# Optimization experiments

Hardware: AMD Instinct MI355X
Metric: run time of the kernel (lower is better)

## Reference

```python
import jax, jax.numpy as jnp
import numpy as np

N_NODES = 100000
N_EDGES = 1600000
IN_DIM, HIDDEN, OUT_DIM = 128, 64, 32
LN_EPS = 1e-5


def setup_inputs() -> dict:
    key = jax.random.key(0)
    ks = jax.random.split(key, 12)
    x = jax.random.normal(ks[0], (N_NODES, IN_DIM), dtype=jnp.float32)
    edge_index = jax.random.randint(ks[1], (2, N_EDGES), 0, N_NODES, dtype=jnp.int64)
    s = 1.0 / np.sqrt(IN_DIM)
    s2 = 1.0 / np.sqrt(HIDDEN)
    return {
        "x": x,
        "edge_index": edge_index,
        "W_self0": jax.random.uniform(ks[2], (IN_DIM, HIDDEN), jnp.float32, -s, s),
        "W_neigh0": jax.random.uniform(ks[3], (IN_DIM, HIDDEN), jnp.float32, -s, s),
        "b0": jnp.zeros((HIDDEN,), jnp.float32),
        "g0": jnp.ones((HIDDEN,), jnp.float32),
        "be0": jnp.zeros((HIDDEN,), jnp.float32),
        "W_self1": jax.random.uniform(ks[4], (HIDDEN, OUT_DIM), jnp.float32, -s2, s2),
        "W_neigh1": jax.random.uniform(ks[5], (HIDDEN, OUT_DIM), jnp.float32, -s2, s2),
        "b1": jnp.zeros((OUT_DIM,), jnp.float32),
        "g1": jnp.ones((OUT_DIM,), jnp.float32),
        "be1": jnp.zeros((OUT_DIM,), jnp.float32),
    }


def _sage_layer(h, src, dst, W_self, W_neigh, b, g, be):
    n = h.shape[0]
    # mean aggregation of neighbor features via scatter-add + count
    agg = jax.ops.segment_sum(h[src], dst, num_segments=n)  # [N, F]
    cnt = jax.ops.segment_sum(jnp.ones((src.shape[0],), h.dtype), dst, num_segments=n)
    agg = agg / jnp.clip(cnt, 1.0)[:, None]
    z = h @ W_self + agg @ W_neigh + b  # [N, out]
    mu = jnp.mean(z, axis=-1, keepdims=True)
    var = jnp.mean((z - mu) ** 2, axis=-1, keepdims=True)
    zn = (z - mu) * jax.lax.rsqrt(var + LN_EPS) * g + be
    return jax.nn.relu(zn)


def reference(x, edge_index, W_self0, W_neigh0, b0, g0, be0,
              W_self1, W_neigh1, b1, g1, be1):
    src, dst = edge_index[0], edge_index[1]
    h = _sage_layer(x, src, dst, W_self0, W_neigh0, b0, g0, be0)
    h = _sage_layer(h, src, dst, W_self1, W_neigh1, b1, g1, be1)
    return h
```

## Files before the change

### kernel.cpp

```cpp
#include <hip/hip_runtime.h>
#include <hip/hip_bf16.h>

#define N_NODES 100000
#define N_EDGES 1600000
#define IN_DIM 128
#define HID 64
#define OUT_DIM 32
#define LN_EPS 1e-5f
#define NBKT 782
#define NPBLK 500
#define PAIRS_PER_BLK 1600
#define G0T 1563
#define PADCAP 384

typedef __attribute__((ext_vector_type(8))) _Float16 half8;
typedef __attribute__((ext_vector_type(8))) short short8;
typedef __attribute__((ext_vector_type(4))) float f32x4;

__device__ __forceinline__ float uflo(unsigned int u) {
  return __uint_as_float(u << 16);
}
__device__ __forceinline__ float ufhi(unsigned int u) {
  return __uint_as_float(u & 0xffff0000u);
}
__device__ __forceinline__ unsigned short bf16rne(float f) {
  unsigned int u = __float_as_uint(f);
  unsigned int r = u + 0x7fffu + ((u >> 16) & 1u);
  return (unsigned short)(r >> 16);
}
__device__ __forceinline__ unsigned int pk(float lo, float hi) {
  return (unsigned int)bf16rne(lo) | ((unsigned int)bf16rne(hi) << 16);
}

__global__ void detect_edges(const int* __restrict__ w, int* __restrict__ flag,
                             unsigned short* __restrict__ p0u,
                             unsigned short* __restrict__ p1u) {
  __shared__ int any;
  if (threadIdx.x == 0) any = 0;
  __syncthreads();
  if (w[2 * threadIdx.x + 1] != 0) any = 1;
  __syncthreads();
  if (threadIdx.x == 0) flag[0] = any ? 0 : 1;
  const int t = threadIdx.x;
  if (t < HID) p0u[(size_t)N_NODES * HID + t] = 0;
  if (t < OUT_DIM) p1u[(size_t)N_NODES * OUT_DIM + t] = 0;
}

__global__ __launch_bounds__(256) void convW(
    const float* __restrict__ Wn0, const float* __restrict__ Ws0,
    const float* __restrict__ Wn1, const float* __restrict__ Ws1,
    _Float16* __restrict__ B0f, unsigned short* __restrict__ B1u) {
  const int i = blockIdx.x * 256 + threadIdx.x;
  if (i < 128 * 128) {
    const int n = i >> 7, k = i & 127;
    const float w = (n < 64) ? Wn0[k * 64 + n] : Ws0[k * 64 + (n - 64)];
    B0f[i] = (_Float16)w;
  } else if (i < 128 * 128 + 64 * 64) {
    const int j = i - 128 * 128;
    const int n = j >> 6, k = j & 63;
    const float w = (n < 32) ? Wn1[k * 32 + n] : Ws1[k * 32 + (n - 32)];
    B1u[j] = bf16rne(w);
  }
}

__device__ __forceinline__ void gemm0_body(
    int rowblk, int colgrp, int tid, _Float16* lb,
    const float* __restrict__ x, const _Float16* __restrict__ B0f,
    const float* __restrict__ b0, unsigned short* __restrict__ p0u,
    unsigned short* __restrict__ s0bu) {
  const int lane = tid & 63;
  const int wave = tid >> 6;
  const int rowbase = rowblk * 64 + wave * 16;
  const int arow = rowbase + (lane & 15);
  const int rclamp = (arow < N_NODES) ? arow : 0;
  const int ko = (lane >> 4) << 3;

  float av[32];
  {
    const float* ax = x + (size_t)rclamp * IN_DIM + ko;
#pragma unroll
    for (int ks = 0; ks < 4; ++ks) {
      *(float4*)&av[ks * 8] = *(const float4*)(ax + ks * 32);
      *(float4*)&av[ks * 8 + 4] = *(const float4*)(ax + ks * 32 + 4);
    }
  }
  {
    const uint4* gsrc = (const uint4*)(B0f + (colgrp << 13));
    for (int i = tid; i < 1024; i += 256) {
      const int o = i << 4;
      const int sw = o ^ (((o >> 8) & 7) << 4);
      *(uint4*)((char*)lb + sw) = gsrc[i];
    }
  }
  __syncthreads();

  half8 ah[4];
#pragma unroll
  for (int ks = 0; ks < 4; ++ks) {
#pragma unroll
    for (int j = 0; j < 8; ++j) ah[ks][j] = (_Float16)av[ks * 8 + j];
  }

  f32x4 acc[4];
#pragma unroll
  for (int ct = 0; ct < 4; ++ct) acc[ct] = (f32x4){0.f, 0.f, 0.f, 0.f};

#pragma unroll
  for (int ks = 0; ks < 4; ++ks) {
    const int kb = ks * 64 + (ko << 1);
#pragma unroll
    for (int ct = 0; ct < 4; ++ct) {
      const int n = ct * 16 + (lane & 15);
      const int boff = (n << 8) + kb;
      const int sb = boff ^ (((boff >> 8) & 7) << 4);
      const half8 bv = *(const half8*)((const char*)lb + sb);
      acc[ct] = __builtin_amdgcn_mfma_f32_16x16x32_f16(ah[ks], bv, acc[ct], 0, 0, 0);
    }
  }
  const int rb4 = rowbase + ((lane >> 4) << 2);
  const int cc = lane & 15;
  if (colgrp == 0) {
#pragma unroll
    for (int ct = 0; ct < 4; ++ct) {
#pragma unroll
      for (int j = 0; j < 4; ++j) {
        const int r = rb4 + j;
        if (r < N_NODES) p0u[(size_t)r * HID + ct * 16 + cc] = bf16rne(acc[ct][j]);
      }
    }
  } else {
#pragma unroll
    for (int ct = 0; ct < 4; ++ct) {
      const float bias = b0[ct * 16 + cc];
#pragma unroll
      for (int j = 0; j < 4; ++j) {
        const int r = rb4 + j;
        if (r < N_NODES)
          s0bu[(size_t)r * HID + ct * 16 + cc] = bf16rne(acc[ct][j] + bias);
      }
    }
  }
}

__global__ __launch_bounds__(256) void fuseA(
    const float* __restrict__ x, const _Float16* __restrict__ B0f,
    const float* __restrict__ b0,
    unsigned short* __restrict__ p0u, unsigned short* __restrict__ s0bu,
    const int* __restrict__ w, const int* __restrict__ flag,
    int* __restrict__ blkbase) {
  __shared__ _Float16 lb[64 * 128];
  const int tid = threadIdx.x;

  if (blockIdx.x < NPBLK) {
    int* h = (int*)lb;
    const int b = blockIdx.x;
    for (int i = tid; i < NBKT; i += 256) h[i] = 0;
    __syncthreads();
    const int i64 = flag[0];
    const int pEnd = (b + 1) * PAIRS_PER_BLK;
    for (int p = b * PAIRS_PER_BLK + tid; p < pEnd; p += 256) {
      int d0, d1;
      if (i64) {
        const int4 vd = *(const int4*)(w + 2 * (size_t)N_EDGES + 4 * (size_t)p);
        d0 = vd.x; d1 = vd.z;
      } else {
        const int2 vd = *(const int2*)(w + (size_t)N_EDGES + 2 * (size_t)p);
        d0 = vd.x; d1 = vd.y;
      }
      atomicAdd(&h[d0 >> 7], 1);
      atomicAdd(&h[d1 >> 7], 1);
    }
    __syncthreads();
    for (int i = tid; i < NBKT; i += 256)
      blkbase[(size_t)b * NBKT + i] = h[i];
    return;
  }
  gemm0_body(blockIdx.x - NPBLK, 0, tid, lb, x, B0f, b0, p0u, s0bu);
}

__global__ __launch_bounds__(256) void bscan(int* __restrict__ blkbase,
                                             int* __restrict__ gcount) {
  __shared__ int lds[256];
  const int i = blockIdx.x;
  const int t = threadIdx.x;
  const int v0 = (t < NPBLK) ? blkbase[(size_t)t * NBKT + i] : 0;
  const int v1 = (t + 256 < NPBLK) ? blkbase[(size_t)(t + 256) * NBKT + i] : 0;
  const int s = v0 + v1;
  lds[t] = s;
  __syncthreads();
  for (int o = 1; o < 256; o <<= 1) {
    const int val = (t >= o) ? lds[t - o] : 0;
    __syncthreads();
    lds[t] += val;
    __syncthreads();
  }
  const int run = lds[t] - s;
  if (t == 255) gcount[i] = lds[255];
  if (t < NPBLK) blkbase[(size_t)t * NBKT + i] = run;
  if (t + 256 < NPBLK) blkbase[(size_t)(t + 256) * NBKT + i] = run + v0;
}

__global__ __launch_bounds__(256) void part_scan(
    const int* __restrict__ gcount, int* __restrict__ gbase) {
  __shared__ int lds[256];
  const int t = threadIdx.x;
  int v[4];
  int s = 0;
#pragma unroll
  for (int j = 0; j < 4; ++j) {
    const int idx = t * 4 + j;
    v[j] = (idx < NBKT) ? gcount[idx] : 0;
    s += v[j];
  }
  lds[t] = s;
  __syncthreads();
  for (int o = 1; o < 256; o <<= 1) {
    const int val = (t >= o) ? lds[t - o] : 0;
    __syncthreads();
    lds[t] += val;
    __syncthreads();
  }
  int run = lds[t] - s;
#pragma unroll
  for (int j = 0; j < 4; ++j) {
    const int idx = t * 4 + j;
    if (idx < NBKT) gbase[idx] = run;
    run += v[j];
  }
}

__global__ __launch_bounds__(256) void fuseB(
    const float* __restrict__ x, const _Float16* __restrict__ B0f,
    const float* __restrict__ b0,
    unsigned short* __restrict__ p0u, unsigned short* __restrict__ s0bu,
    const int* __restrict__ w, const int* __restrict__ flag,
    const int* __restrict__ gbase, const int* __restrict__ blkbase,
    int* __restrict__ pe) {
  __shared__ _Float16 lb[64 * 128];
  const int tid = threadIdx.x;

  if (blockIdx.x < NPBLK) {
    int* cur = (int*)lb;
    const int t = tid, b = blockIdx.x;
    for (int i = t; i < NBKT; i += 256)
      cur[i] = gbase[i] + blkbase[(size_t)b * NBKT + i];
    __syncthreads();
    const int i64 = flag[0];
    const int pEnd = (b + 1) * PAIRS_PER_BLK;
    for (int p = b * PAIRS_PER_BLK + t; p < pEnd; p += 256) {
      int s0, s1, d0, d1;
      if (i64) {
        const int4 vs = *(const int4*)(w + 4 * (size_t)p);
        const int4 vd = *(const int4*)(w + 2 * (size_t)N_EDGES + 4 * (size_t)p);
        s0 = vs.x; s1 = vs.z;
        d0 = vd.x; d1 = vd.z;
      } else {
        const int2 vs = *(const int2*)(w + 2 * (size_t)p);
        const int2 vd = *(const int2*)(w + (size_t)N_EDGES + 2 * (size_t)p);
        s0 = vs.x; s1 = vs.y;
        d0 = vd.x; d1 = vd.y;
      }
      const int sl0 = atomicAdd(&cur[d0 >> 7], 1);
      pe[sl0] = s0 | ((d0 & 127) << 17);
      const int sl1 = atomicAdd(&cur[d1 >> 7], 1);
      pe[sl1] = s1 | ((d1 & 127) << 17);
    }
    return;
  }
  gemm0_body(blockIdx.x - NPBLK, 1, tid, lb, x, B0f, b0, p0u, s0bu);
}

__global__ __launch_bounds__(256) void bucket_csr(
    const int* __restrict__ pe, const int* __restrict__ gbase,
    const int* __restrict__ gcount, int* __restrict__ deg,
    int* __restrict__ off, int* __restrict__ sortedSrc) {
  __shared__ int ldeg[128];
  __shared__ int loff[128];
  __shared__ int lcur[128];
  const int t = threadIdx.x;
  const int bkt = blockIdx.x;
  const int nbase = bkt << 7;
  const int ebase = gbase[bkt];
  const int cnt = gcount[bkt];
  const int outbase = ebase + PADCAP * bkt;
  if (t < 128) ldeg[t] = 0;
  __syncthreads();
  for (int e = t; e < cnt; e += 256) {
    const int pv = pe[ebase + e];
    atomicAdd(&ldeg[(pv >> 17) & 127], 1);
  }
  __syncthreads();
  if (t < 128) loff[t] = (ldeg[t] + 3) & ~3;
  __syncthreads();
  for (int o = 1; o < 128; o <<= 1) {
    int v = 0;
    if (t >= o && t < 128) v = loff[t - o];
    __syncthreads();
    if (t < 128) loff[t] += v;
    __syncthreads();
  }
  if (t < 128) {
    const int pdeg = (ldeg[t] + 3) & ~3;
    const int ex = loff[t] - pdeg;
    lcur[t] = ex;
    const int n = nbase + t;
    if (n < N_NODES) {
      deg[n] = ldeg[t];
      off[n] = outbase + ex;
    }
  }
  __syncthreads();
  for (int e = t; e < cnt; e += 256) {
    const int pv = pe[ebase + e];
    const int ld = (pv >> 17) & 127;
    const int p = atomicAdd(&lcur[ld], 1);
    sortedSrc[outbase + p] = pv & 0x1FFFF;
  }
  __syncthreads();
  if (t < 128) {
    const int pdeg = (ldeg[t] + 3) & ~3;
    const int ex = loff[t] - pdeg;
    for (int q = ldeg[t]; q < pdeg; ++q)
      sortedSrc[outbase + ex + q] = N_NODES;
  }
}

__global__ __launch_bounds__(256) void gemm1(
    const unsigned short* __restrict__ h1u, const unsigned short* __restrict__ B1u,
    const float* __restrict__ b1,
    unsigned short* __restrict__ p1u, unsigned short* __restrict__ s1bu) {
  __shared__ unsigned short lb[64 * 64];
  const int tid = threadIdx.x;
  const int lane = tid & 63;
  const int wave = tid >> 6;
  const int rowbase = blockIdx.x * 64 + wave * 16;
  const int arow = rowbase + (lane & 15);
  const int rclamp = (arow < N_NODES) ? arow : 0;
  const int ko = (lane >> 4) << 3;

  short8 ah[2];
  {
    const unsigned short* ax = h1u + (size_t)rclamp * HID + ko;
    ah[0] = *(const short8*)ax;
    ah[1] = *(const short8*)(ax + 32);
  }
  {
    const uint4* gb = (const uint4*)B1u;
    for (int i = tid; i < 512; i += 256) {
      const int o = i << 4;
      const int sw = o ^ (((o >> 7) & 7) << 4);
      *(uint4*)((char*)lb + sw) = gb[i];
    }
  }
  __syncthreads();

  f32x4 acc[4];
#pragma unroll
  for (int ct = 0; ct < 4; ++ct) acc[ct] = (f32x4){0.f, 0.f, 0.f, 0.f};

#pragma unroll
  for (int ks = 0; ks < 2; ++ks) {
    const int kb = ks * 64 + (ko << 1);
#pragma unroll
    for (int ct = 0; ct < 4; ++ct) {
      const int n = ct * 16 + (lane & 15);
      const int boff = (n << 7) + kb;
      const int sb = boff ^ (((boff >> 7) & 7) << 4);
      const short8 bv = *(const short8*)((const char*)lb + sb);
      acc[ct] = __builtin_amdgcn_mfma_f32_16x16x32_bf16(ah[ks], bv, acc[ct], 0, 0, 0);
    }
  }
  const int rb4 = rowbase + ((lane >> 4) << 2);
  const int cc = lane & 15;
#pragma unroll
  for (int ct = 0; ct < 2; ++ct) {
#pragma unroll
    for (int j = 0; j < 4; ++j) {
      const int r = rb4 + j;
      if (r < N_NODES) p1u[(size_t)r * OUT_DIM + ct * 16 + cc] = bf16rne(acc[ct][j]);
    }
  }
#pragma unroll
  for (int ct = 2; ct < 4; ++ct) {
#pragma unroll
    for (int j = 0; j < 4; ++j) {
      const int r = rb4 + j;
      if (r < N_NODES)
        s1bu[(size_t)r * OUT_DIM + (ct - 2) * 16 + cc] =
            bf16rne(acc[ct][j] + b1[(ct - 2) * 16 + cc]);
    }
  }
}

__global__ __launch_bounds__(256) void aggc0(
    const int* __restrict__ sortedSrc, const int* __restrict__ off,
    const int* __restrict__ deg, const unsigned short* __restrict__ p0u,
    const unsigned short* __restrict__ s0bu, const float* __restrict__ g,
    const float* __restrict__ be, unsigned short* __restrict__ h1u) {
  const int lane = threadIdx.x & 63;
  const int h = lane >> 5;
  const int grp = (lane >> 3) & 3;
  const int sl = lane & 7;
  const int i = blockIdx.x * 8 + ((threadIdx.x >> 6) << 1) + h;
  const int st = off[i];
  const int dg = deg[i];
  const int dgp = (dg + 3) & ~3;
  const int dgmaxp = max(dgp, __shfl_xor(dgp, 32));
  float acc[8];
#pragma unroll
  for (int f = 0; f < 8; ++f) acc[f] = 0.f;

  for (int base = 0; base < dgmaxp; base += 32) {
    const int cntp = dgp - base;
    const int l5 = lane & 31;
    const int idx = (l5 < cntp) ? sortedSrc[st + base + l5] : N_NODES;
    const int cm = min(32, dgmaxp - base);
    for (int j = 0; j * 4 < cm; ++j) {
      const int e = j * 4 + grp;
      const int srcn = __shfl(idx, (h << 5) | e);
      const uint4 q = *(const uint4*)(p0u + (size_t)srcn * HID + sl * 8);
      acc[0] += uflo(q.x); acc[1] += ufhi(q.x);
      acc[2] += uflo(q.y); acc[3] += ufhi(q.y);
      acc[4] += uflo(q.z); acc[5] += ufhi(q.z);
      acc[6] += uflo(q.w); acc[7] += ufhi(q.w);
    }
  }
#pragma unroll
  for (int mk = 8; mk < 32; mk <<= 1) {
#pragma unroll
    for (int f = 0; f < 8; ++f) acc[f] += __shfl_xor(acc[f], mk);
  }
  const float inv = 1.0f / fmaxf((float)dg, 1.0f);
  float z[8];
  const uint4 sbv = *(const uint4*)(s0bu + (size_t)i * HID + sl * 8);
  z[0] = uflo(sbv.x) + acc[0] * inv; z[1] = ufhi(sbv.x) + acc[1] * inv;
  z[2] = uflo(sbv.y) + acc[2] * inv; z[3] = ufhi(sbv.y) + acc[3] * inv;
  z[4] = uflo(sbv.z) + acc[4] * inv; z[5] = ufhi(sbv.z) + acc[5] * inv;
  z[6] = uflo(sbv.w) + acc[6] * inv; z[7] = ufhi(sbv.w) + acc[7] * inv;
  float pm = 0.f;
#pragma unroll
  for (int f = 0; f < 8; ++f) pm += z[f];
#pragma unroll
  for (int mk = 1; mk < 8; mk <<= 1) pm += __shfl_xor(pm, mk);
  const float mean = pm * (1.0f / 64.0f);
  float pv = 0.f;
#pragma unroll
  for (int f = 0; f < 8; ++f) {
    z[f] -= mean;
    pv += z[f] * z[f];
  }
#pragma unroll
  for (int mk = 1; mk < 8; mk <<= 1) pv += __shfl_xor(pv, mk);
  const float rstd = rsqrtf(pv * (1.0f / 64.0f) + LN_EPS);
  if (grp == 0) {
    const float4 gv0 = *(const float4*)(g + sl * 8);
    const float4 gv1 = *(const float4*)(g + sl * 8 + 4);
    const float4 bv0 = *(const float4*)(be + sl * 8);
    const float4 bv1 = *(const float4*)(be + sl * 8 + 4);
    uint4 ov;
    ov.x = pk(fmaxf(z[0] * rstd * gv0.x + bv0.x, 0.f),
              fmaxf(z[1] * rstd * gv0.y + bv0.y, 0.f));
    ov.y = pk(fmaxf(z[2] * rstd * gv0.z + bv0.z, 0.f),
              fmaxf(z[3] * rstd * gv0.w + bv0.w, 0.f));
    ov.z = pk(fmaxf(z[4] * rstd * gv1.x + bv1.x, 0.f),
              fmaxf(z[5] * rstd * gv1.y + bv1.y, 0.f));
    ov.w = pk(fmaxf(z[6] * rstd * gv1.z + bv1.z, 0.f),
              fmaxf(z[7] * rstd * gv1.w + bv1.w, 0.f));
    *(uint4*)(h1u + (size_t)i * HID + sl * 8) = ov;
  }
}

__global__ __launch_bounds__(256) void aggc1(
    const int* __restrict__ sortedSrc, const int* __restrict__ off,
    const int* __restrict__ deg, const unsigned short* __restrict__ p1u,
    const unsigned short* __restrict__ s1bu, const float* __restrict__ g,
    const float* __restrict__ be, float* __restrict__ out) {
  const int lane = threadIdx.x & 63;
  const int q4 = lane >> 4;
  const int grp = (lane >> 2) & 3;
  const int sl = lane & 3;
  const int i = blockIdx.x * 16 + ((threadIdx.x >> 6) << 2) + q4;
  const int st = off[i];
  const int dg = deg[i];
  const int dgp = (dg + 3) & ~3;
  int dm = max(dgp, __shfl_xor(dgp, 16));
  const int dgmaxp = max(dm, __shfl_xor(dm, 32));
  float acc[8];
#pragma unroll
  for (int f = 0; f < 8; ++f) acc[f] = 0.f;

  for (int base = 0; base < dgmaxp; base += 16) {
    const int cntp = dgp - base;
    const int l4 = lane & 15;
    const int idx = (l4 < cntp) ? sortedSrc[st + base + l4] : N_NODES;
    const int cm = min(16, dgmaxp - base);
    for (int j = 0; j * 4 < cm; ++j) {
      const int e = j * 4 + grp;
      const int srcn = __shfl(idx, (q4 << 4) | e);
      const uint4 qv = *(const uint4*)(p1u + (size_t)srcn * OUT_DIM + sl * 8);
      acc[0] += uflo(qv.x); acc[1] += ufhi(qv.x);
      acc[2] += uflo(qv.y); acc[3] += ufhi(qv.y);
      acc[4] += uflo(qv.z); acc[5] += ufhi(qv.z);
      acc[6] += uflo(qv.w); acc[7] += ufhi(qv.w);
    }
  }
#pragma unroll
  for (int mk = 4; mk < 16; mk <<= 1) {
#pragma unroll
    for (int f = 0; f < 8; ++f) acc[f] += __shfl_xor(acc[f], mk);
  }
  const float inv = 1.0f / fmaxf((float)dg, 1.0f);
  float z[8];
  const uint4 sbv = *(const uint4*)(s1bu + (size_t)i * OUT_DIM + sl * 8);
  z[0] = uflo(sbv.x) + acc[0] * inv; z[1] = ufhi(sbv.x) + acc[1] * inv;
  z[2] = uflo(sbv.y) + acc[2] * inv; z[3] = ufhi(sbv.y) + acc[3] * inv;
  z[4] = uflo(sbv.z) + acc[4] * inv; z[5] = ufhi(sbv.z) + acc[5] * inv;
  z[6] = uflo(sbv.w) + acc[6] * inv; z[7] = ufhi(sbv.w) + acc[7] * inv;
  float pm = 0.f;
#pragma unroll
  for (int f = 0; f < 8; ++f) pm += z[f];
#pragma unroll
  for (int mk = 1; mk < 4; mk <<= 1) pm += __shfl_xor(pm, mk);
  const float mean = pm * (1.0f / 32.0f);
  float pv = 0.f;
#pragma unroll
  for (int f = 0; f < 8; ++f) {
    z[f] -= mean;
    pv += z[f] * z[f];
  }
#pragma unroll
  for (int mk = 1; mk < 4; mk <<= 1) pv += __shfl_xor(pv, mk);
  const float rstd = rsqrtf(pv * (1.0f / 32.0f) + LN_EPS);
  if (grp == 0) {
    const float4 gv0 = *(const float4*)(g + sl * 8);
    const float4 gv1 = *(const float4*)(g + sl * 8 + 4);
    const float4 bv0 = *(const float4*)(be + sl * 8);
    const float4 bv1 = *(const float4*)(be + sl * 8 + 4);
    float4 o0, o1;
    o0.x = fmaxf(z[0] * rstd * gv0.x + bv0.x, 0.f);
    o0.y = fmaxf(z[1] * rstd * gv0.y + bv0.y, 0.f);
    o0.z = fmaxf(z[2] * rstd * gv0.z + bv0.z, 0.f);
    o0.w = fmaxf(z[3] * rstd * gv0.w + bv0.w, 0.f);
    o1.x = fmaxf(z[4] * rstd * gv1.x + bv1.x, 0.f);
    o1.y = fmaxf(z[5] * rstd * gv1.y + bv1.y, 0.f);
    o1.z = fmaxf(z[6] * rstd * gv1.z + bv1.z, 0.f);
    o1.w = fmaxf(z[7] * rstd * gv1.w + bv1.w, 0.f);
    *(float4*)(out + (size_t)i * OUT_DIM + sl * 8) = o0;
    *(float4*)(out + (size_t)i * OUT_DIM + sl * 8 + 4) = o1;
  }
}

extern "C" void kernel_launch(void* const* d_in, const int* in_sizes, int n_in,
                              void* d_out, int out_size, void* d_ws, size_t ws_size,
                              hipStream_t stream) {
  const float* x       = (const float*)d_in[0];
  const int*   edges   = (const int*)d_in[1];
  const float* Wself0  = (const float*)d_in[2];
  const float* Wneigh0 = (const float*)d_in[3];
  const float* b0      = (const float*)d_in[4];
  const float* g0      = (const float*)d_in[5];
  const float* be0     = (const float*)d_in[6];
  const float* Wself1  = (const float*)d_in[7];
  const float* Wneigh1 = (const float*)d_in[8];
  const float* b1      = (const float*)d_in[9];
  const float* g1      = (const float*)d_in[10];
  const float* be1     = (const float*)d_in[11];

  char* base = (char*)d_ws;
  size_t o = 0;
  auto carve = [&](size_t bytes) {
    char* p = base + o;
    o += (bytes + 255) & ~(size_t)255;
    return p;
  };
  int* flag      = (int*)carve(64 * 4);
  int* gcount    = (int*)carve(1024 * 4);
  int* gbase     = (int*)carve(1024 * 4);
  int* blkbase   = (int*)carve((size_t)NPBLK * NBKT * 4);
  int* deg       = (int*)carve((size_t)N_NODES * 4);
  int* off       = (int*)carve((size_t)N_NODES * 4);
  int* sortedSrc = (int*)carve(1950000 * 4);
  int* pe        = (int*)carve(6500000);
  _Float16* B0f  = (_Float16*)carve(128 * 128 * 2);
  unsigned short* B1u = (unsigned short*)carve(64 * 64 * 2);
  unsigned short* p0u = (unsigned short*)carve(((size_t)N_NODES + 2) * HID * 2);
  unsigned short* s0bu = (unsigned short*)carve(((size_t)N_NODES + 2) * HID * 2);
  unsigned short* h1u = (unsigned short*)carve(((size_t)N_NODES + 2) * HID * 2);
  unsigned short* p1u = (unsigned short*)pe;
  unsigned short* s1bu = s0bu;

  detect_edges<<<1, 256, 0, stream>>>(edges, flag, p0u, p1u);
  convW<<<80, 256, 0, stream>>>(Wneigh0, Wself0, Wneigh1, Wself1, B0f, B1u);
  fuseA<<<NPBLK + G0T, 256, 0, stream>>>(x, B0f, b0, p0u, s0bu,
                                         edges, flag, blkbase);
  bscan<<<NBKT, 256, 0, stream>>>(blkbase, gcount);
  part_scan<<<1, 256, 0, stream>>>(gcount, gbase);
  fuseB<<<NPBLK + G0T, 256, 0, stream>>>(x, B0f, b0, p0u, s0bu,
                                         edges, flag, gbase, blkbase, pe);
  bucket_csr<<<NBKT, 256, 0, stream>>>(pe, gbase, gcount, deg, off, sortedSrc);

  aggc0<<<N_NODES / 8, 256, 0, stream>>>(sortedSrc, off, deg, p0u, s0bu,
                                         g0, be0, h1u);
  gemm1<<<(N_NODES + 63) / 64, 256, 0, stream>>>(h1u, B1u, b1, p1u, s1bu);
  aggc1<<<N_NODES / 16, 256, 0, stream>>>(sortedSrc, off, deg, p1u, s1bu,
                                          g1, be1, (float*)d_out);
}
```

Baseline: 151.0 us.

## Store layer-0 neighbor projection in FP8 and widen aggregation lanes

The layer-0 neighbor projection is now written as FP8 (one byte per feature) instead of BF16. The aggc0 gather decodes it with packed FP8-to-float conversions, and each lane now handles 16 features. CSR padding rises from multiples of 4 to multiples of 8 to match the new 8-edges-per-step loop, and the padding capacity and sortedSrc buffer grow to fit. The aim is to halve the bytes moved in the random neighbor gather and make the table more cache-resident. In exchange, FP8 rounding of the projected features can hurt accuracy, and the extra padding adds dummy gathers.

```diff
diff --git a/kernel.cpp b/kernel.cpp
--- a/kernel.cpp
+++ b/kernel.cpp
@@ -11,11 +11,12 @@
 #define NPBLK 500
 #define PAIRS_PER_BLK 1600
 #define G0T 1563
-#define PADCAP 384
+#define PADCAP 896
 
 typedef __attribute__((ext_vector_type(8))) _Float16 half8;
 typedef __attribute__((ext_vector_type(8))) short short8;
 typedef __attribute__((ext_vector_type(4))) float f32x4;
+typedef __attribute__((ext_vector_type(2))) float f32x2;
 
 __device__ __forceinline__ float uflo(unsigned int u) {
   return __uint_as_float(u << 16);
@@ -31,9 +32,16 @@
 __device__ __forceinline__ unsigned int pk(float lo, float hi) {
   return (unsigned int)bf16rne(lo) | ((unsigned int)bf16rne(hi) << 16);
 }
+__device__ __forceinline__ unsigned char fp8enc(float v) {
+  return (unsigned char)(__builtin_amdgcn_cvt_pk_fp8_f32(v, 0.f, 0u, false) & 0xff);
+}
+template <bool HI>
+__device__ __forceinline__ f32x2 fp8dec2(unsigned int w) {
+  return __builtin_amdgcn_cvt_pk_f32_fp8(w, HI);
+}
 
 __global__ void detect_edges(const int* __restrict__ w, int* __restrict__ flag,
-                             unsigned short* __restrict__ p0u,
+                             unsigned char* __restrict__ p0f,
                              unsigned short* __restrict__ p1u) {
   __shared__ int any;
   if (threadIdx.x == 0) any = 0;
@@ -42,7 +50,7 @@
   __syncthreads();
   if (threadIdx.x == 0) flag[0] = any ? 0 : 1;
   const int t = threadIdx.x;
-  if (t < HID) p0u[(size_t)N_NODES * HID + t] = 0;
+  if (t < 16) ((unsigned int*)p0f)[(size_t)N_NODES * 16 + t] = 0;
   if (t < OUT_DIM) p1u[(size_t)N_NODES * OUT_DIM + t] = 0;
 }
 
@@ -66,7 +74,7 @@
 __device__ __forceinline__ void gemm0_body(
     int rowblk, int colgrp, int tid, _Float16* lb,
     const float* __restrict__ x, const _Float16* __restrict__ B0f,
-    const float* __restrict__ b0, unsigned short* __restrict__ p0u,
+    const float* __restrict__ b0, unsigned char* __restrict__ p0f,
     unsigned short* __restrict__ s0bu) {
   const int lane = tid & 63;
   const int wave = tid >> 6;
@@ -125,7 +133,7 @@
 #pragma unroll
       for (int j = 0; j < 4; ++j) {
         const int r = rb4 + j;
-        if (r < N_NODES) p0u[(size_t)r * HID + ct * 16 + cc] = bf16rne(acc[ct][j]);
+        if (r < N_NODES) p0f[(size_t)r * HID + ct * 16 + cc] = fp8enc(acc[ct][j]);
       }
     }
   } else {
@@ -145,7 +153,7 @@
 __global__ __launch_bounds__(256) void fuseA(
     const float* __restrict__ x, const _Float16* __restrict__ B0f,
     const float* __restrict__ b0,
-    unsigned short* __restrict__ p0u, unsigned short* __restrict__ s0bu,
+    unsigned char* __restrict__ p0f, unsigned short* __restrict__ s0bu,
     const int* __restrict__ w, const int* __restrict__ flag,
     int* __restrict__ blkbase) {
   __shared__ _Float16 lb[64 * 128];
@@ -175,7 +183,7 @@
       blkbase[(size_t)b * NBKT + i] = h[i];
     return;
   }
-  gemm0_body(blockIdx.x - NPBLK, 0, tid, lb, x, B0f, b0, p0u, s0bu);
+  gemm0_body(blockIdx.x - NPBLK, 0, tid, lb, x, B0f, b0, p0f, s0bu);
 }
 
 __global__ __launch_bounds__(256) void bscan(int* __restrict__ blkbase,
@@ -232,7 +240,7 @@
 __global__ __launch_bounds__(256) void fuseB(
     const float* __restrict__ x, const _Float16* __restrict__ B0f,
     const float* __restrict__ b0,
-    unsigned short* __restrict__ p0u, unsigned short* __restrict__ s0bu,
+    unsigned char* __restrict__ p0f, unsigned short* __restrict__ s0bu,
     const int* __restrict__ w, const int* __restrict__ flag,
     const int* __restrict__ gbase, const int* __restrict__ blkbase,
     int* __restrict__ pe) {
@@ -267,7 +275,7 @@
     }
     return;
   }
-  gemm0_body(blockIdx.x - NPBLK, 1, tid, lb, x, B0f, b0, p0u, s0bu);
+  gemm0_body(blockIdx.x - NPBLK, 1, tid, lb, x, B0f, b0, p0f, s0bu);
 }
 
 __global__ __launch_bounds__(256) void bucket_csr(
@@ -290,7 +298,7 @@
     atomicAdd(&ldeg[(pv >> 17) & 127], 1);
   }
   __syncthreads();
-  if (t < 128) loff[t] = (ldeg[t] + 3) & ~3;
+  if (t < 128) loff[t] = (ldeg[t] + 7) & ~7;
   __syncthreads();
   for (int o = 1; o < 128; o <<= 1) {
     int v = 0;
@@ -300,7 +308,7 @@
     __syncthreads();
   }
   if (t < 128) {
-    const int pdeg = (ldeg[t] + 3) & ~3;
+    const int pdeg = (ldeg[t] + 7) & ~7;
     const int ex = loff[t] - pdeg;
     lcur[t] = ex;
     const int n = nbase + t;
@@ -318,7 +326,7 @@
   }
   __syncthreads();
   if (t < 128) {
-    const int pdeg = (ldeg[t] + 3) & ~3;
+    const int pdeg = (ldeg[t] + 7) & ~7;
     const int ex = loff[t] - pdeg;
     for (int q = ldeg[t]; q < pdeg; ++q)
       sortedSrc[outbase + ex + q] = N_NODES;
@@ -394,79 +402,89 @@
 
 __global__ __launch_bounds__(256) void aggc0(
     const int* __restrict__ sortedSrc, const int* __restrict__ off,
-    const int* __restrict__ deg, const unsigned short* __restrict__ p0u,
+    const int* __restrict__ deg, const unsigned char* __restrict__ p0f,
     const unsigned short* __restrict__ s0bu, const float* __restrict__ g,
     const float* __restrict__ be, unsigned short* __restrict__ h1u) {
   const int lane = threadIdx.x & 63;
   const int h = lane >> 5;
-  const int grp = (lane >> 3) & 3;
-  const int sl = lane & 7;
+  const int grp = (lane >> 2) & 7;
+  const int sl = lane & 3;
   const int i = blockIdx.x * 8 + ((threadIdx.x >> 6) << 1) + h;
   const int st = off[i];
   const int dg = deg[i];
-  const int dgp = (dg + 3) & ~3;
+  const int dgp = (dg + 7) & ~7;
   const int dgmaxp = max(dgp, __shfl_xor(dgp, 32));
-  float acc[8];
-#pragma unroll
-  for (int f = 0; f < 8; ++f) acc[f] = 0.f;
+  float acc[16];
+#pragma unroll
+  for (int f = 0; f < 16; ++f) acc[f] = 0.f;
 
   for (int base = 0; base < dgmaxp; base += 32) {
     const int cntp = dgp - base;
     const int l5 = lane & 31;
     const int idx = (l5 < cntp) ? sortedSrc[st + base + l5] : N_NODES;
     const int cm = min(32, dgmaxp - base);
-    for (int j = 0; j * 4 < cm; ++j) {
-      const int e = j * 4 + grp;
+    for (int j = 0; j * 8 < cm; ++j) {
+      const int e = j * 8 + grp;
       const int srcn = __shfl(idx, (h << 5) | e);
-      const uint4 q = *(const uint4*)(p0u + (size_t)srcn * HID + sl * 8);
-      acc[0] += uflo(q.x); acc[1] += ufhi(q.x);
-      acc[2] += uflo(q.y); acc[3] += ufhi(q.y);
-      acc[4] += uflo(q.z); acc[5] += ufhi(q.z);
-      acc[6] += uflo(q.w); acc[7] += ufhi(q.w);
-    }
-  }
-#pragma unroll
-  for (int mk = 8; mk < 32; mk <<= 1) {
-#pragma unroll
-    for (int f = 0; f < 8; ++f) acc[f] += __shfl_xor(acc[f], mk);
+      const uint4 q = *(const uint4*)(p0f + (size_t)srcn * HID + sl * 16);
+      f32x2 t;
+      t = fp8dec2<false>(q.x); acc[0] += t.x;  acc[1] += t.y;
+      t = fp8dec2<true>(q.x);  acc[2] += t.x;  acc[3] += t.y;
+      t = fp8dec2<false>(q.y); acc[4] += t.x;  acc[5] += t.y;
+      t = fp8dec2<true>(q.y);  acc[6] += t.x;  acc[7] += t.y;
+      t = fp8dec2<false>(q.z); acc[8] += t.x;  acc[9] += t.y;
+      t = fp8dec2<true>(q.z);  acc[10] += t.x; acc[11] += t.y;
+      t = fp8dec2<false>(q.w); acc[12] += t.x; acc[13] += t.y;
+      t = fp8dec2<true>(q.w);  acc[14] += t.x; acc[15] += t.y;
+    }
+  }
+#pragma unroll
+  for (int mk = 4; mk < 32; mk <<= 1) {
+#pragma unroll
+    for (int f = 0; f < 16; ++f) acc[f] += __shfl_xor(acc[f], mk);
   }
   const float inv = 1.0f / fmaxf((float)dg, 1.0f);
-  float z[8];
-  const uint4 sbv = *(const uint4*)(s0bu + (size_t)i * HID + sl * 8);
-  z[0] = uflo(sbv.x) + acc[0] * inv; z[1] = ufhi(sbv.x) + acc[1] * inv;
-  z[2] = uflo(sbv.y) + acc[2] * inv; z[3] = ufhi(sbv.y) + acc[3] * inv;
-  z[4] = uflo(sbv.z) + acc[4] * inv; z[5] = ufhi(sbv.z) + acc[5] * inv;
-  z[6] = uflo(sbv.w) + acc[6] * inv; z[7] = ufhi(sbv.w) + acc[7] * inv;
+  float z[16];
+  const uint4 sb0 = *(const uint4*)(s0bu + (size_t)i * HID + sl * 16);
+  const uint4 sb1 = *(const uint4*)(s0bu + (size_t)i * HID + sl * 16 + 8);
+  z[0] = uflo(sb0.x) + acc[0] * inv;  z[1] = ufhi(sb0.x) + acc[1] * inv;
+  z[2] = uflo(sb0.y) + acc[2] * inv;  z[3] = ufhi(sb0.y) + acc[3] * inv;
+  z[4] = uflo(sb0.z) + acc[4] * inv;  z[5] = ufhi(sb0.z) + acc[5] * inv;
+  z[6] = uflo(sb0.w) + acc[6] * inv;  z[7] = ufhi(sb0.w) + acc[7] * inv;
+  z[8] = uflo(sb1.x) + acc[8] * inv;  z[9] = ufhi(sb1.x) + acc[9] * inv;
+  z[10] = uflo(sb1.y) + acc[10] * inv; z[11] = ufhi(sb1.y) + acc[11] * inv;
+  z[12] = uflo(sb1.z) + acc[12] * inv; z[13] = ufhi(sb1.z) + acc[13] * inv;
+  z[14] = uflo(sb1.w) + acc[14] * inv; z[15] = ufhi(sb1.w) + acc[15] * inv;
   float pm = 0.f;
 #pragma unroll
-  for (int f = 0; f < 8; ++f) pm += z[f];
-#pragma unroll
-  for (int mk = 1; mk < 8; mk <<= 1) pm += __shfl_xor(pm, mk);
+  for (int f = 0; f < 16; ++f) pm += z[f];
+#pragma unroll
+  for (int mk = 1; mk < 4; mk <<= 1) pm += __shfl_xor(pm, mk);
   const float mean = pm * (1.0f / 64.0f);
   float pv = 0.f;
 #pragma unroll
-  for (int f = 0; f < 8; ++f) {
+  for (int f = 0; f < 16; ++f) {
     z[f] -= mean;
     pv += z[f] * z[f];
   }
 #pragma unroll
-  for (int mk = 1; mk < 8; mk <<= 1) pv += __shfl_xor(pv, mk);
+  for (int mk = 1; mk < 4; mk <<= 1) pv += __shfl_xor(pv, mk);
   const float rstd = rsqrtf(pv * (1.0f / 64.0f) + LN_EPS);
   if (grp == 0) {
-    const float4 gv0 = *(const float4*)(g + sl * 8);
-    const float4 gv1 = *(const float4*)(g + sl * 8 + 4);
-    const float4 bv0 = *(const float4*)(be + sl * 8);
-    const float4 bv1 = *(const float4*)(be + sl * 8 + 4);
-    uint4 ov;
-    ov.x = pk(fmaxf(z[0] * rstd * gv0.x + bv0.x, 0.f),
-              fmaxf(z[1] * rstd * gv0.y + bv0.y, 0.f));
-    ov.y = pk(fmaxf(z[2] * rstd * gv0.z + bv0.z, 0.f),
-              fmaxf(z[3] * rstd * gv0.w + bv0.w, 0.f));
-    ov.z = pk(fmaxf(z[4] * rstd * gv1.x + bv1.x, 0.f),
-              fmaxf(z[5] * rstd * gv1.y + bv1.y, 0.f));
-    ov.w = pk(fmaxf(z[6] * rstd * gv1.z + bv1.z, 0.f),
-              fmaxf(z[7] * rstd * gv1.w + bv1.w, 0.f));
-    *(uint4*)(h1u + (size_t)i * HID + sl * 8) = ov;
+    float o16[16];
+#pragma unroll
+    for (int f = 0; f < 16; ++f) {
+      const float gv = g[sl * 16 + f];
+      const float bv = be[sl * 16 + f];
+      o16[f] = fmaxf(z[f] * rstd * gv + bv, 0.f);
+    }
+    uint4 ov0, ov1;
+    ov0.x = pk(o16[0], o16[1]);   ov0.y = pk(o16[2], o16[3]);
+    ov0.z = pk(o16[4], o16[5]);   ov0.w = pk(o16[6], o16[7]);
+    ov1.x = pk(o16[8], o16[9]);   ov1.y = pk(o16[10], o16[11]);
+    ov1.z = pk(o16[12], o16[13]); ov1.w = pk(o16[14], o16[15]);
+    *(uint4*)(h1u + (size_t)i * HID + sl * 16) = ov0;
+    *(uint4*)(h1u + (size_t)i * HID + sl * 16 + 8) = ov1;
   }
 }
 
@@ -579,27 +597,27 @@
   int* blkbase   = (int*)carve((size_t)NPBLK * NBKT * 4);
   int* deg       = (int*)carve((size_t)N_NODES * 4);
   int* off       = (int*)carve((size_t)N_NODES * 4);
-  int* sortedSrc = (int*)carve(1950000 * 4);
+  int* sortedSrc = (int*)carve(2400000 * 4);
   int* pe        = (int*)carve(6500000);
   _Float16* B0f  = (_Float16*)carve(128 * 128 * 2);
   unsigned short* B1u = (unsigned short*)carve(64 * 64 * 2);
-  unsigned short* p0u = (unsigned short*)carve(((size_t)N_NODES + 2) * HID * 2);
+  unsigned char* p0f = (unsigned char*)carve(((size_t)N_NODES + 4) * HID);
   unsigned short* s0bu = (unsigned short*)carve(((size_t)N_NODES + 2) * HID * 2);
   unsigned short* h1u = (unsigned short*)carve(((size_t)N_NODES + 2) * HID * 2);
   unsigned short* p1u = (unsigned short*)pe;
   unsigned short* s1bu = s0bu;
 
-  detect_edges<<<1, 256, 0, stream>>>(edges, flag, p0u, p1u);
+  detect_edges<<<1, 256, 0, stream>>>(edges, flag, p0f, p1u);
   convW<<<80, 256, 0, stream>>>(Wneigh0, Wself0, Wneigh1, Wself1, B0f, B1u);
-  fuseA<<<NPBLK + G0T, 256, 0, stream>>>(x, B0f, b0, p0u, s0bu,
+  fuseA<<<NPBLK + G0T, 256, 0, stream>>>(x, B0f, b0, p0f, s0bu,
                                          edges, flag, blkbase);
   bscan<<<NBKT, 256, 0, stream>>>(blkbase, gcount);
   part_scan<<<1, 256, 0, stream>>>(gcount, gbase);
-  fuseB<<<NPBLK + G0T, 256, 0, stream>>>(x, B0f, b0, p0u, s0bu,
+  fuseB<<<NPBLK + G0T, 256, 0, stream>>>(x, B0f, b0, p0f, s0bu,
                                          edges, flag, gbase, blkbase, pe);
   bucket_csr<<<NBKT, 256, 0, stream>>>(pe, gbase, gcount, deg, off, sortedSrc);
 
-  aggc0<<<N_NODES / 8, 256, 0, stream>>>(sortedSrc, off, deg, p0u, s0bu,
+  aggc0<<<N_NODES / 8, 256, 0, stream>>>(sortedSrc, off, deg, p0f, s0bu,
                                          g0, be0, h1u);
   gemm1<<<(N_NODES + 63) / 64, 256, 0, stream>>>(h1u, B1u, b1, p1u, s1bu);
   aggc1<<<N_NODES / 16, 256, 0, stream>>>(sortedSrc, off, deg, p1u, s1bu,
```

Measured after the change: 152.4 us. Within noise of the previous version (+0.9%).

## Compute both GEMM0 column groups per block and merge setup kernels

Applied to the files above, without the earlier changes.

Each layer-0 GEMM block now computes all 128 output columns (neighbor projection and self+bias) from a single load of its x rows. The row blocks are split between fuseA and fuseB instead of each kernel doing half the columns for every row. This halves the x reads and conversions, at the cost of a larger LDS tile (32KB) and more accumulator registers per block. The edge-detect and weight-conversion kernels are also merged into one launch, saving one launch.

```diff
diff --git a/kernel.cpp b/kernel.cpp
--- a/kernel.cpp
+++ b/kernel.cpp
@@ -10,7 +10,8 @@
 #define NBKT 782
 #define NPBLK 500
 #define PAIRS_PER_BLK 1600
-#define G0T 1563
+#define G0TA 782
+#define G0TB 781
 #define PADCAP 384
 
 typedef __attribute__((ext_vector_type(8))) _Float16 half8;
@@ -32,39 +33,39 @@
   return (unsigned int)bf16rne(lo) | ((unsigned int)bf16rne(hi) << 16);
 }
 
-__global__ void detect_edges(const int* __restrict__ w, int* __restrict__ flag,
-                             unsigned short* __restrict__ p0u,
-                             unsigned short* __restrict__ p1u) {
-  __shared__ int any;
-  if (threadIdx.x == 0) any = 0;
-  __syncthreads();
-  if (w[2 * threadIdx.x + 1] != 0) any = 1;
-  __syncthreads();
-  if (threadIdx.x == 0) flag[0] = any ? 0 : 1;
-  const int t = threadIdx.x;
-  if (t < HID) p0u[(size_t)N_NODES * HID + t] = 0;
-  if (t < OUT_DIM) p1u[(size_t)N_NODES * OUT_DIM + t] = 0;
-}
-
-__global__ __launch_bounds__(256) void convW(
+__global__ __launch_bounds__(256) void detcw(
+    const int* __restrict__ w, int* __restrict__ flag,
     const float* __restrict__ Wn0, const float* __restrict__ Ws0,
     const float* __restrict__ Wn1, const float* __restrict__ Ws1,
-    _Float16* __restrict__ B0f, unsigned short* __restrict__ B1u) {
+    _Float16* __restrict__ B0f, unsigned short* __restrict__ B1u,
+    unsigned short* __restrict__ p0u, unsigned short* __restrict__ p1u) {
+  __shared__ int any;
+  if (blockIdx.x == 80) {
+    if (threadIdx.x == 0) any = 0;
+    __syncthreads();
+    if (w[2 * threadIdx.x + 1] != 0) any = 1;
+    __syncthreads();
+    if (threadIdx.x == 0) flag[0] = any ? 0 : 1;
+    const int t = threadIdx.x;
+    if (t < HID) p0u[(size_t)N_NODES * HID + t] = 0;
+    if (t < OUT_DIM) p1u[(size_t)N_NODES * OUT_DIM + t] = 0;
+    return;
+  }
   const int i = blockIdx.x * 256 + threadIdx.x;
   if (i < 128 * 128) {
     const int n = i >> 7, k = i & 127;
-    const float w = (n < 64) ? Wn0[k * 64 + n] : Ws0[k * 64 + (n - 64)];
-    B0f[i] = (_Float16)w;
+    const float wv = (n < 64) ? Wn0[k * 64 + n] : Ws0[k * 64 + (n - 64)];
+    B0f[i] = (_Float16)wv;
   } else if (i < 128 * 128 + 64 * 64) {
     const int j = i - 128 * 128;
     const int n = j >> 6, k = j & 63;
-    const float w = (n < 32) ? Wn1[k * 32 + n] : Ws1[k * 32 + (n - 32)];
-    B1u[j] = bf16rne(w);
+    const float wv = (n < 32) ? Wn1[k * 32 + n] : Ws1[k * 32 + (n - 32)];
+    B1u[j] = bf16rne(wv);
   }
 }
 
 __device__ __forceinline__ void gemm0_body(
-    int rowblk, int colgrp, int tid, _Float16* lb,
+    int rowblk, int tid, _Float16* lb,
     const float* __restrict__ x, const _Float16* __restrict__ B0f,
     const float* __restrict__ b0, unsigned short* __restrict__ p0u,
     unsigned short* __restrict__ s0bu) {
@@ -85,8 +86,8 @@
     }
   }
   {
-    const uint4* gsrc = (const uint4*)(B0f + (colgrp << 13));
-    for (int i = tid; i < 1024; i += 256) {
+    const uint4* gsrc = (const uint4*)B0f;
+    for (int i = tid; i < 2048; i += 256) {
       const int o = i << 4;
       const int sw = o ^ (((o >> 8) & 7) << 4);
       *(uint4*)((char*)lb + sw) = gsrc[i];
@@ -101,15 +102,15 @@
     for (int j = 0; j < 8; ++j) ah[ks][j] = (_Float16)av[ks * 8 + j];
   }
 
-  f32x4 acc[4];
-#pragma unroll
-  for (int ct = 0; ct < 4; ++ct) acc[ct] = (f32x4){0.f, 0.f, 0.f, 0.f};
+  f32x4 acc[8];
+#pragma unroll
+  for (int ct = 0; ct < 8; ++ct) acc[ct] = (f32x4){0.f, 0.f, 0.f, 0.f};
 
 #pragma unroll
   for (int ks = 0; ks < 4; ++ks) {
     const int kb = ks * 64 + (ko << 1);
 #pragma unroll
-    for (int ct = 0; ct < 4; ++ct) {
+    for (int ct = 0; ct < 8; ++ct) {
       const int n = ct * 16 + (lane & 15);
       const int boff = (n << 8) + kb;
       const int sb = boff ^ (((boff >> 8) & 7) << 4);
@@ -119,25 +120,22 @@
   }
   const int rb4 = rowbase + ((lane >> 4) << 2);
   const int cc = lane & 15;
-  if (colgrp == 0) {
-#pragma unroll
-    for (int ct = 0; ct < 4; ++ct) {
-#pragma unroll
-      for (int j = 0; j < 4; ++j) {
-        const int r = rb4 + j;
-        if (r < N_NODES) p0u[(size_t)r * HID + ct * 16 + cc] = bf16rne(acc[ct][j]);
-      }
-    }
-  } else {
-#pragma unroll
-    for (int ct = 0; ct < 4; ++ct) {
-      const float bias = b0[ct * 16 + cc];
-#pragma unroll
-      for (int j = 0; j < 4; ++j) {
-        const int r = rb4 + j;
-        if (r < N_NODES)
-          s0bu[(size_t)r * HID + ct * 16 + cc] = bf16rne(acc[ct][j] + bias);
-      }
+#pragma unroll
+  for (int ct = 0; ct < 4; ++ct) {
+#pragma unroll
+    for (int j = 0; j < 4; ++j) {
+      const int r = rb4 + j;
+      if (r < N_NODES) p0u[(size_t)r * HID + ct * 16 + cc] = bf16rne(acc[ct][j]);
+    }
+  }
+#pragma unroll
+  for (int ct = 4; ct < 8; ++ct) {
+    const float bias = b0[(ct - 4) * 16 + cc];
+#pragma unroll
+    for (int j = 0; j < 4; ++j) {
+      const int r = rb4 + j;
+      if (r < N_NODES)
+        s0bu[(size_t)r * HID + (ct - 4) * 16 + cc] = bf16rne(acc[ct][j] + bias);
     }
   }
 }
@@ -148,7 +146,7 @@
     unsigned short* __restrict__ p0u, unsigned short* __restrict__ s0bu,
     const int* __restrict__ w, const int* __restrict__ flag,
     int* __restrict__ blkbase) {
-  __shared__ _Float16 lb[64 * 128];
+  __shared__ _Float16 lb[128 * 128];
   const int tid = threadIdx.x;
 
   if (blockIdx.x < NPBLK) {
@@ -175,7 +173,7 @@
       blkbase[(size_t)b * NBKT + i] = h[i];
     return;
   }
-  gemm0_body(blockIdx.x - NPBLK, 0, tid, lb, x, B0f, b0, p0u, s0bu);
+  gemm0_body(blockIdx.x - NPBLK, tid, lb, x, B0f, b0, p0u, s0bu);
 }
 
 __global__ __launch_bounds__(256) void bscan(int* __restrict__ blkbase,
@@ -236,7 +234,7 @@
     const int* __restrict__ w, const int* __restrict__ flag,
     const int* __restrict__ gbase, const int* __restrict__ blkbase,
     int* __restrict__ pe) {
-  __shared__ _Float16 lb[64 * 128];
+  __shared__ _Float16 lb[128 * 128];
   const int tid = threadIdx.x;
 
   if (blockIdx.x < NPBLK) {
@@ -267,7 +265,7 @@
     }
     return;
   }
-  gemm0_body(blockIdx.x - NPBLK, 1, tid, lb, x, B0f, b0, p0u, s0bu);
+  gemm0_body(blockIdx.x - NPBLK + G0TA, tid, lb, x, B0f, b0, p0u, s0bu);
 }
 
 __global__ __launch_bounds__(256) void bucket_csr(
@@ -589,14 +587,14 @@
   unsigned short* p1u = (unsigned short*)pe;
   unsigned short* s1bu = s0bu;
 
-  detect_edges<<<1, 256, 0, stream>>>(edges, flag, p0u, p1u);
-  convW<<<80, 256, 0, stream>>>(Wneigh0, Wself0, Wneigh1, Wself1, B0f, B1u);
-  fuseA<<<NPBLK + G0T, 256, 0, stream>>>(x, B0f, b0, p0u, s0bu,
-                                         edges, flag, blkbase);
+  detcw<<<81, 256, 0, stream>>>(edges, flag, Wneigh0, Wself0, Wneigh1, Wself1,
+                                B0f, B1u, p0u, p1u);
+  fuseA<<<NPBLK + G0TA, 256, 0, stream>>>(x, B0f, b0, p0u, s0bu,
+                                          edges, flag, blkbase);
   bscan<<<NBKT, 256, 0, stream>>>(blkbase, gcount);
   part_scan<<<1, 256, 0, stream>>>(gcount, gbase);
-  fuseB<<<NPBLK + G0T, 256, 0, stream>>>(x, B0f, b0, p0u, s0bu,
-                                         edges, flag, gbase, blkbase, pe);
+  fuseB<<<NPBLK + G0TB, 256, 0, stream>>>(x, B0f, b0, p0u, s0bu,
+                                          edges, flag, gbase, blkbase, pe);
   bucket_csr<<<NBKT, 256, 0, stream>>>(pe, gbase, gcount, deg, off, sortedSrc);
 
   aggc0<<<N_NODES / 8, 256, 0, stream>>>(sortedSrc, off, deg, p0u, s0bu,
```

New measurement: 146.1 us. 3.3% less time.
